# Optimization experiments

Hardware: AMD Instinct MI355X
Metric: run time of the kernel (lower is better)

The kernel has to match this reference:

```python
import jax, jax.numpy as jnp
import numpy as np

N_NODES = 100000
N_EDGES = 1600000
IN, HID, OUT = 128, 256, 64
EPS = 0.0  # init_eps=0, learn_eps=False


def setup_inputs() -> dict:
    key = jax.random.key(0)
    k1, k2, k3, k4, k5 = jax.random.split(key, 5)
    x = jax.random.normal(k1, (N_NODES, IN), dtype=jnp.float32)
    edge_src = jax.random.randint(k2, (N_EDGES,), 0, N_NODES, dtype=jnp.int64)
    edge_dst = jax.random.randint(k3, (N_EDGES,), 0, N_NODES, dtype=jnp.int64)
    W1 = jax.random.normal(k4, (IN, HID), dtype=jnp.float32) * (1.0 / np.sqrt(IN))
    W2 = jax.random.normal(k5, (HID, OUT), dtype=jnp.float32) * (1.0 / np.sqrt(HID))
    return {"x": x, "edge_src": edge_src, "edge_dst": edge_dst, "W1": W1, "W2": W2}


def _gin_conv(h, edge_src, edge_dst, W, n_nodes):
    # sum aggregation of messages h[src] into dst, then (1+eps)*h + agg, then linear (no bias)
    agg = jax.ops.segment_sum(h[edge_src], edge_dst, num_segments=n_nodes)
    return ((1.0 + EPS) * h + agg) @ W


def reference(x, edge_src, edge_dst, W1, W2):
    n = x.shape[0]
    h = _gin_conv(x, edge_src, edge_dst, W1, n)   # [N, HID]
    h = _gin_conv(h, edge_src, edge_dst, W2, n)   # [N, OUT]
    return h
```

## Files before the change

### kernel.cpp

```cpp
#include <hip/hip_runtime.h>
#include <hip/hip_bf16.h>

#define IN_F  128
#define HID_F 256
#define OUT_F 64
#define BUCKET_SHIFT 9
#define BUCKET_SZ 512
#define EPB 4096
#define CAP 10240

typedef __attribute__((ext_vector_type(8))) short bf16x8;
typedef __attribute__((ext_vector_type(4))) float f32x4;

__device__ __forceinline__ float bf2f(unsigned short u) {
    union { unsigned int i; float f; } v; v.i = ((unsigned int)u) << 16; return v.f;
}
__device__ __forceinline__ float bf2f_lo(unsigned int p) {
    union { unsigned int i; float f; } v; v.i = p << 16; return v.f;
}
__device__ __forceinline__ float bf2f_hi(unsigned int p) {
    union { unsigned int i; float f; } v; v.i = p & 0xffff0000u; return v.f;
}
__device__ __forceinline__ unsigned short f2bf(float f) {
    __hip_bfloat16 b = __float2bfloat16(f);
    return *reinterpret_cast<unsigned short*>(&b);
}

__global__ __launch_bounds__(256) void k_front(
    const float* __restrict__ x, unsigned short* __restrict__ xb, long long total8,
    const float* __restrict__ W1, const float* __restrict__ W2,
    unsigned short* __restrict__ w12s, int xBlocks)
{
    int bid = blockIdx.x;
    int t = threadIdx.x;
    if (bid < xBlocks) {
        long long i = (long long)bid * 256 + t;
        if (i >= total8) return;
        const float4* p = reinterpret_cast<const float4*>(x) + i * 2;
        float4 a = p[0], b = p[1];
        ushort4 o0, o1;
        o0.x = f2bf(a.x); o0.y = f2bf(a.y); o0.z = f2bf(a.z); o0.w = f2bf(a.w);
        o1.x = f2bf(b.x); o1.y = f2bf(b.y); o1.z = f2bf(b.z); o1.w = f2bf(b.w);
        reinterpret_cast<ushort4*>(xb)[i * 2]     = o0;
        reinterpret_cast<ushort4*>(xb)[i * 2 + 1] = o1;
    } else {
        int idx = (bid - xBlocks) * 256 + t;
        int c = idx >> 9, L = (idx >> 3) & 63, j = idx & 7;
        int nt = c >> 2, ks = c & 3;
        int k = ks * 32 + (L >> 4) * 8 + j;
        int n = nt * 16 + (L & 15);
        float s = 0.f;
        #pragma unroll 8
        for (int jj = 0; jj < HID_F; ++jj)
            s += W1[k * HID_F + jj] * W2[jj * OUT_F + n];
        w12s[idx] = f2bf(s);
    }
}

__global__ __launch_bounds__(1024) void k_bin(
    const int* __restrict__ src, const int* __restrict__ dst,
    int* __restrict__ gcur, unsigned int* __restrict__ binned, int nEdges)
{
    __shared__ int hist[256];
    __shared__ int lcur[256];
    int t = threadIdx.x;
    if (t < 256) hist[t] = 0;
    __syncthreads();
    long long base = (long long)blockIdx.x * EPB;
    #pragma unroll
    for (int k = 0; k < EPB / 1024; ++k) {
        long long e = base + k * 1024 + t;
        if (e < nEdges) atomicAdd(&hist[dst[e] >> BUCKET_SHIFT], 1);
    }
    __syncthreads();
    if (t < 256) {
        int h = hist[t];
        lcur[t] = (h > 0) ? atomicAdd(&gcur[t], h) : 0;
    }
    __syncthreads();
    #pragma unroll
    for (int k = 0; k < EPB / 1024; ++k) {
        long long e = base + k * 1024 + t;
        if (e < nEdges) {
            int s = src[e], d = dst[e];
            int b = d >> BUCKET_SHIFT;
            int pos = atomicAdd(&lcur[b], 1);
            binned[(size_t)b * CAP + pos] =
                (((unsigned int)(d & (BUCKET_SZ - 1))) << 23) | (unsigned int)s;
        }
    }
}

__global__ __launch_bounds__(512) void k_localcsr(
    const unsigned int* __restrict__ binned, const int* __restrict__ gcur,
    int* __restrict__ rowbeg, int* __restrict__ rowend,
    int* __restrict__ eidx, int nNodes)
{
    __shared__ int ldeg[BUCKET_SZ];
    __shared__ int lscan[BUCKET_SZ];
    int t = threadIdx.x;
    ldeg[t] = 0;
    __syncthreads();
    int eb0 = blockIdx.x * CAP;
    int cnt = gcur[blockIdx.x];
    int node0 = blockIdx.x << BUCKET_SHIFT;
    for (int e = t; e < cnt; e += 512)
        atomicAdd(&ldeg[binned[eb0 + e] >> 23], 1);
    __syncthreads();
    int s = ldeg[t];
    lscan[t] = s;
    __syncthreads();
    for (int d = 1; d < 512; d <<= 1) {
        int add = (t >= d) ? lscan[t - d] : 0;
        __syncthreads();
        lscan[t] += add;
        __syncthreads();
    }
    int excl = lscan[t] - s;
    int n0 = node0 + t;
    if (n0 < nNodes) { rowbeg[n0] = eb0 + excl; rowend[n0] = eb0 + excl + s; }
    __syncthreads();
    ldeg[t] = excl;
    __syncthreads();
    for (int e = t; e < cnt; e += 512) {
        unsigned int p = binned[eb0 + e];
        int dl = (int)(p >> 23), sv = (int)(p & 0x7fffffu);
        int pos = atomicAdd(&ldeg[dl], 1);
        eidx[eb0 + pos] = sv;
    }
}

__global__ __launch_bounds__(1024) void gather1z(
    const unsigned short* __restrict__ xb, const int* __restrict__ rowbeg,
    const int* __restrict__ rowend, const int* __restrict__ eidx,
    const unsigned short* __restrict__ w12s,
    unsigned short* __restrict__ z, int nNodes)
{
    __shared__ unsigned short aggT[16 * IN_F];
    int wave = threadIdx.x >> 6, lane = threadIdx.x & 63;
    int m0 = blockIdx.x * 16;
    int n = m0 + wave;
    int g = lane >> 4;
    int f = lane & 15;
    char* sc = reinterpret_cast<char*>(aggT);

    if (n < nNodes) {
        int beg = __builtin_amdgcn_readfirstlane(rowbeg[n]);
        int end = __builtin_amdgcn_readfirstlane(rowend[n]);
        float acc[8] = {0.f, 0.f, 0.f, 0.f, 0.f, 0.f, 0.f, 0.f};
        for (int e0 = beg; e0 < end; e0 += 64) {
            int cnt = min(64, end - e0);
            int e = (lane < cnt) ? eidx[e0 + lane] : 0;
            for (int i = 0; i < cnt; i += 16) {
                uint4 v[4];
                unsigned int vmask[4];
                #pragma unroll
                for (int j = 0; j < 4; ++j) {
                    int eij = i + 4 * j + g;
                    int src = __builtin_amdgcn_ds_bpermute(eij << 2, e);
                    int s0  = __builtin_amdgcn_readlane(e, i + 4 * j);
                    bool valid = eij < cnt;
                    vmask[j] = valid ? 0xffffffffu : 0u;
                    src = valid ? src : s0;
                    v[j] = *reinterpret_cast<const uint4*>(
                        xb + (unsigned)src * IN_F + (f << 3));
                }
                #pragma unroll
                for (int j = 0; j < 4; ++j) {
                    unsigned int a0 = v[j].x & vmask[j], a1 = v[j].y & vmask[j];
                    unsigned int a2 = v[j].z & vmask[j], a3 = v[j].w & vmask[j];
                    acc[0] += bf2f_lo(a0); acc[1] += bf2f_hi(a0);
                    acc[2] += bf2f_lo(a1); acc[3] += bf2f_hi(a1);
                    acc[4] += bf2f_lo(a2); acc[5] += bf2f_hi(a2);
                    acc[6] += bf2f_lo(a3); acc[7] += bf2f_hi(a3);
                }
            }
        }
        #pragma unroll
        for (int k = 0; k < 8; ++k) {
            acc[k] += __shfl_xor(acc[k], 16);
            acc[k] += __shfl_xor(acc[k], 32);
        }
        uint4 sv = *reinterpret_cast<const uint4*>(xb + (size_t)n * IN_F + (f << 3));
        acc[0] += bf2f_lo(sv.x); acc[1] += bf2f_hi(sv.x);
        acc[2] += bf2f_lo(sv.y); acc[3] += bf2f_hi(sv.y);
        acc[4] += bf2f_lo(sv.z); acc[5] += bf2f_hi(sv.z);
        acc[6] += bf2f_lo(sv.w); acc[7] += bf2f_hi(sv.w);
        if (g == 0) {
            uint4 o;
            o.x = (unsigned int)f2bf(acc[0]) | ((unsigned int)f2bf(acc[1]) << 16);
            o.y = (unsigned int)f2bf(acc[2]) | ((unsigned int)f2bf(acc[3]) << 16);
            o.z = (unsigned int)f2bf(acc[4]) | ((unsigned int)f2bf(acc[5]) << 16);
            o.w = (unsigned int)f2bf(acc[6]) | ((unsigned int)f2bf(acc[7]) << 16);
            int b = ((wave << 8) + (f << 4)) ^ ((wave & 7) << 4);
            *reinterpret_cast<uint4*>(sc + b) = o;
        }
    } else {
        if (g == 0) {
            int b = ((wave << 8) + (f << 4)) ^ ((wave & 7) << 4);
            *reinterpret_cast<uint4*>(sc + b) = make_uint4(0, 0, 0, 0);
        }
    }
    __syncthreads();

    if (wave < 4) {
        int row = lane & 15, quad = lane >> 4;
        f32x4 acc2 = {};
        const bf16x8* bBase = reinterpret_cast<const bf16x8*>(w12s) + lane;
        #pragma unroll
        for (int ks = 0; ks < 4; ++ks) {
            int ab = ((row << 8) + (quad << 4) + (ks << 6)) ^ ((row & 7) << 4);
            bf16x8 a = *reinterpret_cast<const bf16x8*>(sc + ab);
            bf16x8 b = bBase[(wave * 4 + ks) * 64];
            acc2 = __builtin_amdgcn_mfma_f32_16x16x32_bf16(a, b, acc2, 0, 0, 0);
        }
        size_t outBase = (size_t)(m0 + quad * 4) * OUT_F + wave * 16 + row;
        #pragma unroll
        for (int i = 0; i < 4; ++i) {
            if (m0 + quad * 4 + i >= nNodes) break;
            z[outBase + (size_t)i * OUT_F] = f2bf(acc2[i]);
        }
    }
}

__global__ __launch_bounds__(256) void gather2(
    const unsigned short* __restrict__ z, const int* __restrict__ rowbeg,
    const int* __restrict__ rowend,
    const int* __restrict__ eidx, float* __restrict__ out, int nNodes)
{
    int n    = blockIdx.x * 4 + __builtin_amdgcn_readfirstlane(threadIdx.x >> 6);
    int lane = threadIdx.x & 63;
    if (n >= nNodes) return;
    int beg = __builtin_amdgcn_readfirstlane(rowbeg[n]);
    int end = __builtin_amdgcn_readfirstlane(rowend[n]);
    int g = lane >> 3;
    int f = lane & 7;
    float acc[8] = {0.f, 0.f, 0.f, 0.f, 0.f, 0.f, 0.f, 0.f};

    for (int e0 = beg; e0 < end; e0 += 64) {
        int cnt = min(64, end - e0);
        int e = (lane < cnt) ? eidx[e0 + lane] : 0;
        for (int i = 0; i < cnt; i += 32) {
            uint4 v[4];
            unsigned int vmask[4];
            #pragma unroll
            for (int j = 0; j < 4; ++j) {
                int eij = i + 8 * j + g;
                int src = __builtin_amdgcn_ds_bpermute(eij << 2, e);
                int s0  = __builtin_amdgcn_readlane(e, i + 8 * j);
                bool valid = eij < cnt;
                vmask[j] = valid ? 0xffffffffu : 0u;
                src = valid ? src : s0;
                v[j] = *reinterpret_cast<const uint4*>(
                    z + (unsigned)src * OUT_F + (f << 3));
            }
            #pragma unroll
            for (int j = 0; j < 4; ++j) {
                unsigned int a0 = v[j].x & vmask[j], a1 = v[j].y & vmask[j];
                unsigned int a2 = v[j].z & vmask[j], a3 = v[j].w & vmask[j];
                acc[0] += bf2f_lo(a0); acc[1] += bf2f_hi(a0);
                acc[2] += bf2f_lo(a1); acc[3] += bf2f_hi(a1);
                acc[4] += bf2f_lo(a2); acc[5] += bf2f_hi(a2);
                acc[6] += bf2f_lo(a3); acc[7] += bf2f_hi(a3);
            }
        }
    }
    #pragma unroll
    for (int k = 0; k < 8; ++k) {
        acc[k] += __shfl_xor(acc[k], 8);
        acc[k] += __shfl_xor(acc[k], 16);
        acc[k] += __shfl_xor(acc[k], 32);
    }
    uint4 sv = *reinterpret_cast<const uint4*>(z + (size_t)n * OUT_F + (f << 3));
    acc[0] += bf2f_lo(sv.x); acc[1] += bf2f_hi(sv.x);
    acc[2] += bf2f_lo(sv.y); acc[3] += bf2f_hi(sv.y);
    acc[4] += bf2f_lo(sv.z); acc[5] += bf2f_hi(sv.z);
    acc[6] += bf2f_lo(sv.w); acc[7] += bf2f_hi(sv.w);
    if (g == 0) {
        float* o = out + (size_t)n * OUT_F + (f << 3);
        *reinterpret_cast<float4*>(o)     = make_float4(acc[0], acc[1], acc[2], acc[3]);
        *reinterpret_cast<float4*>(o + 4) = make_float4(acc[4], acc[5], acc[6], acc[7]);
    }
}

extern "C" void kernel_launch(void* const* d_in, const int* in_sizes, int n_in,
                              void* d_out, int out_size, void* d_ws, size_t ws_size,
                              hipStream_t stream) {
    const float* x  = (const float*)d_in[0];
    const int* esrc = (const int*)d_in[1];
    const int* edst = (const int*)d_in[2];
    const float* W1 = (const float*)d_in[3];
    const float* W2 = (const float*)d_in[4];
    float* out      = (float*)d_out;

    const int nNodes = in_sizes[0] / IN_F;
    const int nEdges = in_sizes[1];
    const int NB = (nNodes + BUCKET_SZ - 1) / BUCKET_SZ;
    const int A  = (nEdges + EPB - 1) / EPB;

    char* ws = (char*)d_ws;
    size_t off = 0;
    auto alloc = [&](size_t bytes) {
        char* p = ws + off; off = (off + bytes + 63) & ~(size_t)63; return p;
    };
    unsigned short* xb  = (unsigned short*)alloc((size_t)nNodes * IN_F * 2);
    unsigned short* z   = (unsigned short*)alloc((size_t)nNodes * OUT_F * 2);
    unsigned int* binned = (unsigned int*)alloc((size_t)NB * CAP * 4);
    int* eidx           = (int*)alloc((size_t)NB * CAP * 4);
    unsigned short* w12s = (unsigned short*)alloc((size_t)IN_F * OUT_F * 2);
    int* rowbeg         = (int*)alloc((size_t)nNodes * 4);
    int* rowend         = (int*)alloc((size_t)nNodes * 4);
    int* gcur           = (int*)alloc(256 * 4);

    hipMemsetAsync(gcur, 0, 256 * 4, stream);

    long long total8 = (long long)nNodes * IN_F / 8;
    const int xBlocks = (int)((total8 + 255) / 256);
    k_front<<<xBlocks + 32, 256, 0, stream>>>(
        x, xb, total8, W1, W2, w12s, xBlocks);

    k_bin<<<A, 1024, 0, stream>>>(esrc, edst, gcur, binned, nEdges);
    k_localcsr<<<NB, 512, 0, stream>>>(binned, gcur, rowbeg, rowend, eidx, nNodes);

    const int g1Blocks = (nNodes + 15) / 16;
    const int nBlocks = (nNodes + 3) / 4;
    gather1z<<<g1Blocks, 1024, 0, stream>>>(xb, rowbeg, rowend, eidx, w12s, z, nNodes);
    gather2<<<nBlocks, 256, 0, stream>>>(z, rowbeg, rowend, eidx, out, nNodes);
}
```

Before: 255.9 us.

## Fuse front conversion with edge binning; give each gather1z wave four rows

Merges the x-to-bf16 conversion, W1·W2 precompute and edge binning into one 1024-thread launch, removing a kernel launch and letting the independent work overlap. gather1z now handles 64 nodes per block, with each wave aggregating 4 rows in sequence. All 16 waves then run MFMA on four 16-row tiles instead of only 4 waves doing so. The block count drops fourfold, but each wave's aggregation becomes serial over 4 nodes, which lowers in-flight gather parallelism per wave and can worsen load imbalance.

Result: slower. 262.4 us (+2.6%).

```diff
diff --git a/kernel.cpp b/kernel.cpp
--- a/kernel.cpp
+++ b/kernel.cpp
@@ -26,15 +26,20 @@
     return *reinterpret_cast<unsigned short*>(&b);
 }
 
-__global__ __launch_bounds__(256) void k_front(
+__global__ __launch_bounds__(1024) void k_front_bin(
     const float* __restrict__ x, unsigned short* __restrict__ xb, long long total8,
     const float* __restrict__ W1, const float* __restrict__ W2,
-    unsigned short* __restrict__ w12s, int xBlocks)
+    unsigned short* __restrict__ w12s,
+    const int* __restrict__ esrc, const int* __restrict__ edst,
+    int* __restrict__ gcur, unsigned int* __restrict__ binned,
+    int nEdges, int xBlocks)
 {
+    __shared__ int hist[256];
+    __shared__ int lcur[256];
     int bid = blockIdx.x;
     int t = threadIdx.x;
     if (bid < xBlocks) {
-        long long i = (long long)bid * 256 + t;
+        long long i = (long long)bid * 1024 + t;
         if (i >= total8) return;
         const float4* p = reinterpret_cast<const float4*>(x) + i * 2;
         float4 a = p[0], b = p[1];
@@ -43,8 +48,8 @@
         o1.x = f2bf(b.x); o1.y = f2bf(b.y); o1.z = f2bf(b.z); o1.w = f2bf(b.w);
         reinterpret_cast<ushort4*>(xb)[i * 2]     = o0;
         reinterpret_cast<ushort4*>(xb)[i * 2 + 1] = o1;
-    } else {
-        int idx = (bid - xBlocks) * 256 + t;
+    } else if (bid < xBlocks + 8) {
+        int idx = (bid - xBlocks) * 1024 + t;
         int c = idx >> 9, L = (idx >> 3) & 63, j = idx & 7;
         int nt = c >> 2, ks = c & 3;
         int k = ks * 32 + (L >> 4) * 8 + j;
@@ -54,39 +59,32 @@
         for (int jj = 0; jj < HID_F; ++jj)
             s += W1[k * HID_F + jj] * W2[jj * OUT_F + n];
         w12s[idx] = f2bf(s);
-    }
-}
-
-__global__ __launch_bounds__(1024) void k_bin(
-    const int* __restrict__ src, const int* __restrict__ dst,
-    int* __restrict__ gcur, unsigned int* __restrict__ binned, int nEdges)
-{
-    __shared__ int hist[256];
-    __shared__ int lcur[256];
-    int t = threadIdx.x;
-    if (t < 256) hist[t] = 0;
-    __syncthreads();
-    long long base = (long long)blockIdx.x * EPB;
-    #pragma unroll
-    for (int k = 0; k < EPB / 1024; ++k) {
-        long long e = base + k * 1024 + t;
-        if (e < nEdges) atomicAdd(&hist[dst[e] >> BUCKET_SHIFT], 1);
-    }
-    __syncthreads();
-    if (t < 256) {
-        int h = hist[t];
-        lcur[t] = (h > 0) ? atomicAdd(&gcur[t], h) : 0;
-    }
-    __syncthreads();
-    #pragma unroll
-    for (int k = 0; k < EPB / 1024; ++k) {
-        long long e = base + k * 1024 + t;
-        if (e < nEdges) {
-            int s = src[e], d = dst[e];
-            int b = d >> BUCKET_SHIFT;
-            int pos = atomicAdd(&lcur[b], 1);
-            binned[(size_t)b * CAP + pos] =
-                (((unsigned int)(d & (BUCKET_SZ - 1))) << 23) | (unsigned int)s;
+    } else {
+        int bb = bid - xBlocks - 8;
+        if (t < 256) hist[t] = 0;
+        __syncthreads();
+        long long base = (long long)bb * EPB;
+        #pragma unroll
+        for (int k = 0; k < EPB / 1024; ++k) {
+            long long e = base + k * 1024 + t;
+            if (e < nEdges) atomicAdd(&hist[edst[e] >> BUCKET_SHIFT], 1);
+        }
+        __syncthreads();
+        if (t < 256) {
+            int h = hist[t];
+            lcur[t] = (h > 0) ? atomicAdd(&gcur[t], h) : 0;
+        }
+        __syncthreads();
+        #pragma unroll
+        for (int k = 0; k < EPB / 1024; ++k) {
+            long long e = base + k * 1024 + t;
+            if (e < nEdges) {
+                int s = esrc[e], d = edst[e];
+                int b = d >> BUCKET_SHIFT;
+                int pos = atomicAdd(&lcur[b], 1);
+                binned[(size_t)b * CAP + pos] =
+                    (((unsigned int)(d & (BUCKET_SZ - 1))) << 23) | (unsigned int)s;
+            }
         }
     }
 }
@@ -136,74 +134,78 @@
     const unsigned short* __restrict__ w12s,
     unsigned short* __restrict__ z, int nNodes)
 {
-    __shared__ unsigned short aggT[16 * IN_F];
+    __shared__ unsigned short aggT[64 * IN_F];
     int wave = threadIdx.x >> 6, lane = threadIdx.x & 63;
-    int m0 = blockIdx.x * 16;
-    int n = m0 + wave;
+    int m0 = blockIdx.x * 64;
     int g = lane >> 4;
     int f = lane & 15;
-    char* sc = reinterpret_cast<char*>(aggT);
-
-    if (n < nNodes) {
-        int beg = __builtin_amdgcn_readfirstlane(rowbeg[n]);
-        int end = __builtin_amdgcn_readfirstlane(rowend[n]);
-        float acc[8] = {0.f, 0.f, 0.f, 0.f, 0.f, 0.f, 0.f, 0.f};
-        for (int e0 = beg; e0 < end; e0 += 64) {
-            int cnt = min(64, end - e0);
-            int e = (lane < cnt) ? eidx[e0 + lane] : 0;
-            for (int i = 0; i < cnt; i += 16) {
-                uint4 v[4];
-                unsigned int vmask[4];
-                #pragma unroll
-                for (int j = 0; j < 4; ++j) {
-                    int eij = i + 4 * j + g;
-                    int src = __builtin_amdgcn_ds_bpermute(eij << 2, e);
-                    int s0  = __builtin_amdgcn_readlane(e, i + 4 * j);
-                    bool valid = eij < cnt;
-                    vmask[j] = valid ? 0xffffffffu : 0u;
-                    src = valid ? src : s0;
-                    v[j] = *reinterpret_cast<const uint4*>(
-                        xb + (unsigned)src * IN_F + (f << 3));
+    char* scb = reinterpret_cast<char*>(aggT);
+
+    for (int j = 0; j < 4; ++j) {
+        int r = wave * 4 + j;
+        int n = m0 + r;
+        char* sc = scb + ((r >> 4) << 12);
+        int lr = r & 15;
+        int wb = ((lr << 8) + (f << 4)) ^ ((lr & 7) << 4);
+        if (n < nNodes) {
+            int beg = __builtin_amdgcn_readfirstlane(rowbeg[n]);
+            int end = __builtin_amdgcn_readfirstlane(rowend[n]);
+            float acc[8] = {0.f, 0.f, 0.f, 0.f, 0.f, 0.f, 0.f, 0.f};
+            for (int e0 = beg; e0 < end; e0 += 64) {
+                int cnt = min(64, end - e0);
+                int e = (lane < cnt) ? eidx[e0 + lane] : 0;
+                for (int i = 0; i < cnt; i += 16) {
+                    uint4 v[4];
+                    unsigned int vmask[4];
+                    #pragma unroll
+                    for (int jj = 0; jj < 4; ++jj) {
+                        int eij = i + 4 * jj + g;
+                        int src = __builtin_amdgcn_ds_bpermute(eij << 2, e);
+                        int s0  = __builtin_amdgcn_readlane(e, i + 4 * jj);
+                        bool valid = eij < cnt;
+                        vmask[jj] = valid ? 0xffffffffu : 0u;
+                        src = valid ? src : s0;
+                        v[jj] = *reinterpret_cast<const uint4*>(
+                            xb + (unsigned)src * IN_F + (f << 3));
+                    }
+                    #pragma unroll
+                    for (int jj = 0; jj < 4; ++jj) {
+                        unsigned int a0 = v[jj].x & vmask[jj], a1 = v[jj].y & vmask[jj];
+                        unsigned int a2 = v[jj].z & vmask[jj], a3 = v[jj].w & vmask[jj];
+                        acc[0] += bf2f_lo(a0); acc[1] += bf2f_hi(a0);
+                        acc[2] += bf2f_lo(a1); acc[3] += bf2f_hi(a1);
+                        acc[4] += bf2f_lo(a2); acc[5] += bf2f_hi(a2);
+                        acc[6] += bf2f_lo(a3); acc[7] += bf2f_hi(a3);
+                    }
                 }
-                #pragma unroll
-                for (int j = 0; j < 4; ++j) {
-                    unsigned int a0 = v[j].x & vmask[j], a1 = v[j].y & vmask[j];
-                    unsigned int a2 = v[j].z & vmask[j], a3 = v[j].w & vmask[j];
-                    acc[0] += bf2f_lo(a0); acc[1] += bf2f_hi(a0);
-                    acc[2] += bf2f_lo(a1); acc[3] += bf2f_hi(a1);
-                    acc[4] += bf2f_lo(a2); acc[5] += bf2f_hi(a2);
-                    acc[6] += bf2f_lo(a3); acc[7] += bf2f_hi(a3);
-                }
-            }
-        }
-        #pragma unroll
-        for (int k = 0; k < 8; ++k) {
-            acc[k] += __shfl_xor(acc[k], 16);
-            acc[k] += __shfl_xor(acc[k], 32);
-        }
-        uint4 sv = *reinterpret_cast<const uint4*>(xb + (size_t)n * IN_F + (f << 3));
-        acc[0] += bf2f_lo(sv.x); acc[1] += bf2f_hi(sv.x);
-        acc[2] += bf2f_lo(sv.y); acc[3] += bf2f_hi(sv.y);
-        acc[4] += bf2f_lo(sv.z); acc[5] += bf2f_hi(sv.z);
-        acc[6] += bf2f_lo(sv.w); acc[7] += bf2f_hi(sv.w);
-        if (g == 0) {
-            uint4 o;
-            o.x = (unsigned int)f2bf(acc[0]) | ((unsigned int)f2bf(acc[1]) << 16);
-            o.y = (unsigned int)f2bf(acc[2]) | ((unsigned int)f2bf(acc[3]) << 16);
-            o.z = (unsigned int)f2bf(acc[4]) | ((unsigned int)f2bf(acc[5]) << 16);
-            o.w = (unsigned int)f2bf(acc[6]) | ((unsigned int)f2bf(acc[7]) << 16);
-            int b = ((wave << 8) + (f << 4)) ^ ((wave & 7) << 4);
-            *reinterpret_cast<uint4*>(sc + b) = o;
-        }
-    } else {
-        if (g == 0) {
-            int b = ((wave << 8) + (f << 4)) ^ ((wave & 7) << 4);
-            *reinterpret_cast<uint4*>(sc + b) = make_uint4(0, 0, 0, 0);
-        }
-    }
-    __syncthreads();
-
-    if (wave < 4) {
+            }
+            #pragma unroll
+            for (int k = 0; k < 8; ++k) {
+                acc[k] += __shfl_xor(acc[k], 16);
+                acc[k] += __shfl_xor(acc[k], 32);
+            }
+            uint4 sv = *reinterpret_cast<const uint4*>(xb + (size_t)n * IN_F + (f << 3));
+            acc[0] += bf2f_lo(sv.x); acc[1] += bf2f_hi(sv.x);
+            acc[2] += bf2f_lo(sv.y); acc[3] += bf2f_hi(sv.y);
+            acc[4] += bf2f_lo(sv.z); acc[5] += bf2f_hi(sv.z);
+            acc[6] += bf2f_lo(sv.w); acc[7] += bf2f_hi(sv.w);
+            if (g == 0) {
+                uint4 o;
+                o.x = (unsigned int)f2bf(acc[0]) | ((unsigned int)f2bf(acc[1]) << 16);
+                o.y = (unsigned int)f2bf(acc[2]) | ((unsigned int)f2bf(acc[3]) << 16);
+                o.z = (unsigned int)f2bf(acc[4]) | ((unsigned int)f2bf(acc[5]) << 16);
+                o.w = (unsigned int)f2bf(acc[6]) | ((unsigned int)f2bf(acc[7]) << 16);
+                *reinterpret_cast<uint4*>(sc + wb) = o;
+            }
+        } else {
+            if (g == 0) *reinterpret_cast<uint4*>(sc + wb) = make_uint4(0, 0, 0, 0);
+        }
+    }
+    __syncthreads();
+
+    {
+        int tile = wave >> 2, nt = wave & 3;
+        char* sc = scb + (tile << 12);
         int row = lane & 15, quad = lane >> 4;
         f32x4 acc2 = {};
         const bf16x8* bBase = reinterpret_cast<const bf16x8*>(w12s) + lane;
@@ -211,13 +213,14 @@
         for (int ks = 0; ks < 4; ++ks) {
             int ab = ((row << 8) + (quad << 4) + (ks << 6)) ^ ((row & 7) << 4);
             bf16x8 a = *reinterpret_cast<const bf16x8*>(sc + ab);
-            bf16x8 b = bBase[(wave * 4 + ks) * 64];
+            bf16x8 b = bBase[(nt * 4 + ks) * 64];
             acc2 = __builtin_amdgcn_mfma_f32_16x16x32_bf16(a, b, acc2, 0, 0, 0);
         }
-        size_t outBase = (size_t)(m0 + quad * 4) * OUT_F + wave * 16 + row;
+        int mt = m0 + tile * 16;
+        size_t outBase = (size_t)(mt + quad * 4) * OUT_F + nt * 16 + row;
         #pragma unroll
         for (int i = 0; i < 4; ++i) {
-            if (m0 + quad * 4 + i >= nNodes) break;
+            if (mt + quad * 4 + i >= nNodes) break;
             z[outBase + (size_t)i * OUT_F] = f2bf(acc2[i]);
         }
     }
@@ -315,14 +318,13 @@
     hipMemsetAsync(gcur, 0, 256 * 4, stream);
 
     long long total8 = (long long)nNodes * IN_F / 8;
-    const int xBlocks = (int)((total8 + 255) / 256);
-    k_front<<<xBlocks + 32, 256, 0, stream>>>(
-        x, xb, total8, W1, W2, w12s, xBlocks);
-
-    k_bin<<<A, 1024, 0, stream>>>(esrc, edst, gcur, binned, nEdges);
+    const int xBlocks = (int)((total8 + 1023) / 1024);
+    k_front_bin<<<xBlocks + 8 + A, 1024, 0, stream>>>(
+        x, xb, total8, W1, W2, w12s, esrc, edst, gcur, binned, nEdges, xBlocks);
+
     k_localcsr<<<NB, 512, 0, stream>>>(binned, gcur, rowbeg, rowend, eidx, nNodes);
 
-    const int g1Blocks = (nNodes + 15) / 16;
+    const int g1Blocks = (nNodes + 63) / 64;
     const int nBlocks = (nNodes + 3) / 4;
     gather1z<<<g1Blocks, 1024, 0, stream>>>(xb, rowbeg, rowend, eidx, w12s, z, nNodes);
     gather2<<<nBlocks, 256, 0, stream>>>(z, rowbeg, rowend, eidx, out, nNodes);
```
